# Kernel tuning notes

Measured on AMD Instinct MI355X. Metric: run time of the kernel, lower is better.

The kernel has to match this reference:

```python
import jax, jax.numpy as jnp
import numpy as np

BS = 8192
INPUT_DIM = 4096
LAYER_DIMS = [64, 256, 64]
BLOCK_DIM = LAYER_DIMS[0]
N_BLOCKS = INPUT_DIM // BLOCK_DIM


def setup_inputs() -> dict:
    key = jax.random.key(0)
    kx, kw1, kw2 = jax.random.split(key, 3)
    x = jax.random.normal(kx, (BS, INPUT_DIM), dtype=jnp.float32)
    # BlockLinear params: weight ~ randn, bias ~ zeros (as in torch source)
    W1 = jax.random.normal(kw1, (N_BLOCKS, LAYER_DIMS[0], LAYER_DIMS[1]), dtype=jnp.float32)
    b1 = jnp.zeros((N_BLOCKS, 1, LAYER_DIMS[1]), dtype=jnp.float32)
    W2 = jax.random.normal(kw2, (N_BLOCKS, LAYER_DIMS[1], LAYER_DIMS[2]), dtype=jnp.float32)
    b2 = jnp.zeros((N_BLOCKS, 1, LAYER_DIMS[2]), dtype=jnp.float32)
    return {"x": x, "W1": W1, "b1": b1, "W2": W2, "b2": b2}


def reference(x, W1, b1, W2, b2):
    bs = x.shape[0]
    # [bs, input_dim] -> [n_blocks, bs, block_dim]
    h = x.reshape(bs, N_BLOCKS, BLOCK_DIM).transpose(1, 0, 2)
    # BlockLinear 1 (bmm + bias) then exact GELU (torch nn.GELU default)
    h = jnp.einsum('nbi,nio->nbo', h, W1) + b1
    h = jax.nn.gelu(h, approximate=False)
    # BlockLinear 2
    h = jnp.einsum('nbi,nio->nbo', h, W2) + b2
    # [n_blocks, bs, out_block] -> [bs, n_blocks*out_block]
    return h.transpose(1, 0, 2).reshape(bs, -1)
```

## Files before the change

kernel.cpp:

```cpp
#include <hip/hip_runtime.h>

using f16x8 = _Float16 __attribute__((ext_vector_type(8)));
using f32x4 = float __attribute__((ext_vector_type(4)));

#define BS      8192
#define IN_DIM  4096
#define NB      64
#define BD      64
#define HID     256
#define OD      64
#define GY      32

__device__ __forceinline__ float gelu_f(float z) {
    float t = z * z;
    float p = __builtin_fmaf(0.044715f * z, t, z);
    float e = __builtin_amdgcn_exp2f(p * 2.3021193f);
    float r = __builtin_amdgcn_rcpf(e + 1.0f);
    return __builtin_fmaf(-z, r, z);
}

__global__ __launch_bounds__(512, 4) void blockmlp_kernel(
    const float* __restrict__ xg, const float* __restrict__ w1g,
    const float* __restrict__ b1g, const float* __restrict__ w2g,
    const float* __restrict__ b2g, float* __restrict__ outg) {

    __shared__ _Float16 W1T[HID * BD];
    __shared__ _Float16 W2L[2048 * 8];
    __shared__ float    b1L[HID];

    const int tid = threadIdx.x;
    const int w   = tid >> 6;
    const int l   = tid & 63;
    const int g   = l >> 4;
    const int l15 = l & 15;
    const int n   = blockIdx.x;

    const float* W1n = w1g + (size_t)n * (BD * HID);
    #pragma unroll
    for (int it = 0; it < 32; ++it) {
        int e = tid + it * 512;
        int i = e >> 8;
        int o = e & 255;
        W1T[(o * 64 + i) ^ ((o & 7) << 3)] = (_Float16)W1n[e];
    }

    const float* W2n = w2g + (size_t)n * (HID * OD);
    #pragma unroll
    for (int i4 = 0; i4 < 4; ++i4) {
        int e  = tid * 4 + i4;
        int p  = e >> 8;
        int n2 = (e >> 6) & 3;
        int le = e & 63;
        int ge = le >> 4, ce = le & 15;
        f16x8 v;
        #pragma unroll
        for (int j = 0; j < 8; ++j)
            v[j] = (_Float16)W2n[(size_t)(p * 32 + ((j >> 2) << 4) + ge * 4 + (j & 3)) * 64 + n2 * 16 + ce];
        *(f16x8*)&W2L[e * 8] = v;
    }

    if (tid < HID) b1L[tid] = b1g[n * HID + tid];

    float b2b[4];
    #pragma unroll
    for (int n2 = 0; n2 < 4; ++n2) b2b[n2] = b2g[n * OD + n2 * 16 + l15];

    __syncthreads();

    const int row0 = blockIdx.y * 256 + w * 32;

    f16x8 xa[2][2];
    #pragma unroll
    for (int rs = 0; rs < 2; ++rs)
        #pragma unroll
        for (int ks = 0; ks < 2; ++ks) {
            const float* px = xg + (size_t)(row0 + rs * 16 + l15) * IN_DIM + n * BD + ks * 32 + g * 8;
            float4 lo = *(const float4*)px;
            float4 hi = *(const float4*)(px + 4);
            f16x8 v;
            v[0] = (_Float16)lo.x; v[1] = (_Float16)lo.y;
            v[2] = (_Float16)lo.z; v[3] = (_Float16)lo.w;
            v[4] = (_Float16)hi.x; v[5] = (_Float16)hi.y;
            v[6] = (_Float16)hi.z; v[7] = (_Float16)hi.w;
            xa[rs][ks] = v;
        }

    const f32x4 z4 = {0.0f, 0.0f, 0.0f, 0.0f};
    f32x4 c2[2][4];
    #pragma unroll
    for (int rs = 0; rs < 2; ++rs)
        #pragma unroll
        for (int n2 = 0; n2 < 4; ++n2) c2[rs][n2] = z4;

    const int swz = (l15 & 7) << 3;

    #pragma unroll
    for (int p = 0; p < 8; ++p) {
        f32x4 c1[2][2];
        #pragma unroll
        for (int htl = 0; htl < 2; ++htl) {
            const int o = (p * 2 + htl) * 16 + l15;
            f32x4 ca = z4, cb = z4;
            #pragma unroll
            for (int ks = 0; ks < 2; ++ks) {
                f16x8 wf = *(const f16x8*)&W1T[o * 64 + ((ks * 32 + g * 8) ^ swz)];
                ca = __builtin_amdgcn_mfma_f32_16x16x32_f16(wf, xa[0][ks], ca, 0, 0, 0);
                cb = __builtin_amdgcn_mfma_f32_16x16x32_f16(wf, xa[1][ks], cb, 0, 0, 0);
            }
            c1[htl][0] = ca; c1[htl][1] = cb;
        }
        f32x4 b1a = *(const f32x4*)&b1L[(p * 2 + 0) * 16 + g * 4];
        f32x4 b1b = *(const f32x4*)&b1L[(p * 2 + 1) * 16 + g * 4];
        f16x8 a2[2];
        #pragma unroll
        for (int rs = 0; rs < 2; ++rs) {
            f16x8 v;
            #pragma unroll
            for (int q = 0; q < 4; ++q) {
                v[q]     = (_Float16)gelu_f(c1[0][rs][q] + b1a[q]);
                v[q + 4] = (_Float16)gelu_f(c1[1][rs][q] + b1b[q]);
            }
            a2[rs] = v;
        }
        #pragma unroll
        for (int n2 = 0; n2 < 4; ++n2) {
            f16x8 bf = *(const f16x8*)&W2L[((p * 4 + n2) * 64 + l) * 8];
            c2[0][n2] = __builtin_amdgcn_mfma_f32_16x16x32_f16(a2[0], bf, c2[0][n2], 0, 0, 0);
            c2[1][n2] = __builtin_amdgcn_mfma_f32_16x16x32_f16(a2[1], bf, c2[1][n2], 0, 0, 0);
        }
    }

    #pragma unroll
    for (int rs = 0; rs < 2; ++rs)
        #pragma unroll
        for (int n2 = 0; n2 < 4; ++n2)
            #pragma unroll
            for (int q = 0; q < 4; ++q) {
                int row = row0 + rs * 16 + g * 4 + q;
                outg[(size_t)row * IN_DIM + n * BD + n2 * 16 + l15] = c2[rs][n2][q] + b2b[n2];
            }
}

extern "C" void kernel_launch(void* const* d_in, const int* in_sizes, int n_in,
                              void* d_out, int out_size, void* d_ws, size_t ws_size,
                              hipStream_t stream) {
    const float* x  = (const float*)d_in[0];
    const float* W1 = (const float*)d_in[1];
    const float* b1 = (const float*)d_in[2];
    const float* W2 = (const float*)d_in[3];
    const float* b2 = (const float*)d_in[4];
    float* out = (float*)d_out;

    dim3 grid(NB, GY, 1);
    dim3 block(512, 1, 1);
    hipLaunchKernelGGL(blockmlp_kernel, grid, block, 0, stream, x, W1, b1, W2, b2, out);
}
```

Measured before the change: 78.46 us.

## Double block size to 1024 threads and pre-swizzle W1 into MFMA fragment layout

Each workgroup now has 1024 threads covering 512 rows, which halves the grid in Y and halves how often each workgroup's W1/W2 blocks are staged into LDS. W1 is stored in LDS in the exact per-lane MFMA fragment order, replacing the transposed XOR-swizzled layout, so each lane reads one contiguous 16-byte vector. The output store loop is reordered so row addressing is computed once per row. Launch bounds now ask for 1024 threads with 8 waves per EU, which tightens the register budget and may cause spills; the gathered global reads for W1 are strided.

```diff
diff --git a/kernel.cpp b/kernel.cpp
--- a/kernel.cpp
+++ b/kernel.cpp
@@ -9,7 +9,7 @@
 #define BD      64
 #define HID     256
 #define OD      64
-#define GY      32
+#define GY      16
 
 __device__ __forceinline__ float gelu_f(float z) {
     float t = z * z;
@@ -19,12 +19,12 @@
     return __builtin_fmaf(-z, r, z);
 }
 
-__global__ __launch_bounds__(512, 4) void blockmlp_kernel(
+__global__ __launch_bounds__(1024, 8) void blockmlp_kernel(
     const float* __restrict__ xg, const float* __restrict__ w1g,
     const float* __restrict__ b1g, const float* __restrict__ w2g,
     const float* __restrict__ b2g, float* __restrict__ outg) {
 
-    __shared__ _Float16 W1T[HID * BD];
+    __shared__ _Float16 W1F[2048 * 8];
     __shared__ _Float16 W2L[2048 * 8];
     __shared__ float    b1L[HID];
 
@@ -37,17 +37,23 @@
 
     const float* W1n = w1g + (size_t)n * (BD * HID);
     #pragma unroll
-    for (int it = 0; it < 32; ++it) {
-        int e = tid + it * 512;
-        int i = e >> 8;
-        int o = e & 255;
-        W1T[(o * 64 + i) ^ ((o & 7) << 3)] = (_Float16)W1n[e];
+    for (int i2 = 0; i2 < 2; ++i2) {
+        int e  = i2 * 1024 + tid;
+        int ht = e >> 7;
+        int ks = (e >> 6) & 1;
+        int le = e & 63;
+        int ge = le >> 4, oo = le & 15;
+        f16x8 v;
+        #pragma unroll
+        for (int j = 0; j < 8; ++j)
+            v[j] = (_Float16)W1n[(size_t)(ks * 32 + ge * 8 + j) * HID + ht * 16 + oo];
+        *(f16x8*)&W1F[e * 8] = v;
     }
 
     const float* W2n = w2g + (size_t)n * (HID * OD);
     #pragma unroll
-    for (int i4 = 0; i4 < 4; ++i4) {
-        int e  = tid * 4 + i4;
+    for (int i2 = 0; i2 < 2; ++i2) {
+        int e  = i2 * 1024 + tid;
         int p  = e >> 8;
         int n2 = (e >> 6) & 3;
         int le = e & 63;
@@ -55,7 +61,7 @@
         f16x8 v;
         #pragma unroll
         for (int j = 0; j < 8; ++j)
-            v[j] = (_Float16)W2n[(size_t)(p * 32 + ((j >> 2) << 4) + ge * 4 + (j & 3)) * 64 + n2 * 16 + ce];
+            v[j] = (_Float16)W2n[(size_t)(p * 32 + ((j >> 2) << 4) + ge * 4 + (j & 3)) * OD + n2 * 16 + ce];
         *(f16x8*)&W2L[e * 8] = v;
     }
 
@@ -67,7 +73,8 @@
 
     __syncthreads();
 
-    const int row0 = blockIdx.y * 256 + w * 32;
+    const int row0 = blockIdx.y * 512 + w * 32;
+    const f32x4 z4 = {0.0f, 0.0f, 0.0f, 0.0f};
 
     f16x8 xa[2][2];
     #pragma unroll
@@ -85,25 +92,21 @@
             xa[rs][ks] = v;
         }
 
-    const f32x4 z4 = {0.0f, 0.0f, 0.0f, 0.0f};
     f32x4 c2[2][4];
     #pragma unroll
     for (int rs = 0; rs < 2; ++rs)
         #pragma unroll
         for (int n2 = 0; n2 < 4; ++n2) c2[rs][n2] = z4;
 
-    const int swz = (l15 & 7) << 3;
-
     #pragma unroll
     for (int p = 0; p < 8; ++p) {
         f32x4 c1[2][2];
         #pragma unroll
         for (int htl = 0; htl < 2; ++htl) {
-            const int o = (p * 2 + htl) * 16 + l15;
             f32x4 ca = z4, cb = z4;
             #pragma unroll
             for (int ks = 0; ks < 2; ++ks) {
-                f16x8 wf = *(const f16x8*)&W1T[o * 64 + ((ks * 32 + g * 8) ^ swz)];
+                f16x8 wf = *(const f16x8*)&W1F[((((p * 2 + htl) * 2) + ks) * 64 + l) * 8];
                 ca = __builtin_amdgcn_mfma_f32_16x16x32_f16(wf, xa[0][ks], ca, 0, 0, 0);
                 cb = __builtin_amdgcn_mfma_f32_16x16x32_f16(wf, xa[1][ks], cb, 0, 0, 0);
             }
@@ -133,12 +136,13 @@
     #pragma unroll
     for (int rs = 0; rs < 2; ++rs)
         #pragma unroll
-        for (int n2 = 0; n2 < 4; ++n2)
+        for (int q = 0; q < 4; ++q) {
+            int row = row0 + rs * 16 + g * 4 + q;
+            float* po = outg + (size_t)row * IN_DIM + n * BD + l15;
             #pragma unroll
-            for (int q = 0; q < 4; ++q) {
-                int row = row0 + rs * 16 + g * 4 + q;
-                outg[(size_t)row * IN_DIM + n * BD + n2 * 16 + l15] = c2[rs][n2][q] + b2b[n2];
-            }
+            for (int n2 = 0; n2 < 4; ++n2)
+                po[n2 * 16] = c2[rs][n2][q] + b2b[n2];
+        }
 }
 
 extern "C" void kernel_launch(void* const* d_in, const int* in_sizes, int n_in,
@@ -152,6 +156,6 @@
     float* out = (float*)d_out;
 
     dim3 grid(NB, GY, 1);
-    dim3 block(512, 1, 1);
+    dim3 block(1024, 1, 1);
     hipLaunchKernelGGL(blockmlp_kernel, grid, block, 0, stream, x, W1, b1, W2, b2, out);
 }
```

Result: slower. 167.8 us (+113.8%).
